# Kernel tuning notes

Measured on AMD Instinct MI355X. Metric: run time of the kernel, lower is better.

Reference implementation:

```python
import jax, jax.numpy as jnp
import numpy as np

IN_CH = 512
EMB = 512

def setup_inputs() -> dict:
    key = jax.random.key(0)
    ks = jax.random.split(key, 14)
    s = 0.02
    inp = {
        'input': jax.random.normal(ks[0], (8, IN_CH, 64, 64), jnp.float32),
        'context': jax.random.normal(ks[1], (8, EMB, 32, 32), jnp.float32),
        # proj_in: Conv2d(in_channels, emb_dim, 1) -> weight [emb, in_ch]
        'proj_in_w': jax.random.normal(ks[2], (EMB, IN_CH), jnp.float32) * s,
        'proj_in_b': jnp.zeros((EMB,), jnp.float32),
        # Linear weights stored as [in, out] (math-equivalent to torch [out,in].T)
        'wq_w': jax.random.normal(ks[3], (EMB, EMB), jnp.float32) * s,
        'wq_b': jnp.zeros((EMB,), jnp.float32),
        'wk_w': jax.random.normal(ks[4], (EMB, EMB), jnp.float32) * s,
        'wk_b': jnp.zeros((EMB,), jnp.float32),
        'wv_w': jax.random.normal(ks[5], (EMB, EMB), jnp.float32) * s,
        'wv_b': jnp.zeros((EMB,), jnp.float32),
        # proj_out: Conv2d(emb+in_ch, in_ch, 1) -> weight [in_ch, emb+in_ch]
        'proj_out_w': jax.random.normal(ks[6], (IN_CH, EMB + IN_CH), jnp.float32) * s,
        'proj_out_b': jnp.zeros((IN_CH,), jnp.float32),
    }
    return inp

def reference(input, context, proj_in_w, proj_in_b, wq_w, wq_b, wk_w, wk_b,
              wv_w, wv_b, proj_out_w, proj_out_b):
    b, c_in, h, w = input.shape
    _, c_ctx, hc, wc = context.shape
    scale = EMB ** (-0.5)

    # context: [b, emb, hc, wc] -> [b, L, emb]
    ctx = context.reshape(b, c_ctx, hc * wc).transpose(0, 2, 1)

    # proj_in (1x1 conv) + flatten: [b, in_ch, h, w] -> [b, hw, emb]
    x = jnp.einsum('bchw,ec->bhwe', input, proj_in_w) + proj_in_b
    x = x.reshape(b, h * w, EMB)

    Q = x @ wq_w + wq_b                 # [b, hw, emb]
    K = ctx @ wk_w + wk_b               # [b, L, emb]
    V = ctx @ wv_w + wv_b               # [b, L, emb]

    att = jnp.einsum('bid,bjd->bij', Q, K) * scale  # [b, hw, L]
    att = jax.nn.softmax(att, axis=-1)
    out = jnp.einsum('bij,bjd->bid', att, V)        # [b, hw, emb]

    # [b, hw, emb] -> [b, emb, h, w]
    out = out.reshape(b, h, w, EMB).transpose(0, 3, 1, 2)
    out = jnp.concatenate([input, out], axis=1)     # [b, in_ch+emb, h, w]
    out = jnp.einsum('bchw,oc->bohw', out, proj_out_w) + proj_out_b[None, :, None, None]
    return out
```

## Files before the change

### kernel.cpp

```cpp
#include <hip/hip_runtime.h>
#include <hip/hip_bf16.h>

using bf16 = __hip_bfloat16;
typedef short s16x8 __attribute__((ext_vector_type(8)));
typedef float f32x4 __attribute__((ext_vector_type(4)));
typedef unsigned short u16;

__device__ __forceinline__ void gld_lds16(const void* g, void* l) {
  __builtin_amdgcn_global_load_lds(
      (const __attribute__((address_space(1))) void*)g,
      (__attribute__((address_space(3))) void*)l, 16, 0, 0);
}

__device__ __forceinline__ float bf2f(u16 u) {
  unsigned int x = ((unsigned int)u) << 16;
  return __builtin_bit_cast(float, x);
}

__global__ __launch_bounds__(256) void convert_f32_bf16(
    const float* __restrict__ in, bf16* __restrict__ out, int n) {
  int i = blockIdx.x * 256 + threadIdx.x;
  if (i < n) out[i] = __float2bfloat16(in[i]);
}

__global__ __launch_bounds__(256) void zero_f32(float* __restrict__ p, int n) {
  int i = blockIdx.x * 256 + threadIdx.x;
  if (i < n) p[i] = 0.f;
}

__global__ __launch_bounds__(256) void transpose_f32_to_bf16(
    const float* __restrict__ in, bf16* __restrict__ out, int inner,
    long in_b, long out_b, int out_ld, int coloff) {
  __shared__ float tile[32][33];
  const int bx = blockIdx.x;
  const int by = blockIdx.y;
  const int bz = blockIdx.z;
  const int tx = threadIdx.x & 31;
  const int ty = threadIdx.x >> 5;
  const float* ib = in + (long)bz * in_b;
  bf16* ob = out + (long)bz * out_b;
#pragma unroll
  for (int i = 0; i < 4; ++i) {
    int r = ty + i * 8;
    tile[r][tx] = ib[(long)(by * 32 + r) * inner + bx * 32 + tx];
  }
  __syncthreads();
#pragma unroll
  for (int i = 0; i < 4; ++i) {
    int r = ty + i * 8;
    ob[(long)(bx * 32 + r) * out_ld + coloff + by * 32 + tx] =
        __float2bfloat16(tile[tx][r]);
  }
}

__global__ __launch_bounds__(256) void transpose_w4(
    const float* __restrict__ w0, const float* __restrict__ w1,
    const float* __restrict__ w2, const float* __restrict__ w3,
    bf16* __restrict__ o0, bf16* __restrict__ o1,
    bf16* __restrict__ o2, bf16* __restrict__ o3) {
  __shared__ float tile[32][33];
  const float* in;
  bf16* out;
  switch (blockIdx.z) {
    case 0: in = w0; out = o0; break;
    case 1: in = w1; out = o1; break;
    case 2: in = w2; out = o2; break;
    default: in = w3; out = o3; break;
  }
  const int bx = blockIdx.x, by = blockIdx.y;
  const int tx = threadIdx.x & 31, ty = threadIdx.x >> 5;
#pragma unroll
  for (int i = 0; i < 4; ++i) {
    int r = ty + i * 8;
    tile[r][tx] = in[(long)(by * 32 + r) * 512 + bx * 32 + tx];
  }
  __syncthreads();
#pragma unroll
  for (int i = 0; i < 4; ++i) {
    int r = ty + i * 8;
    out[(long)(bx * 32 + r) * 512 + by * 32 + tx] = __float2bfloat16(tile[tx][r]);
  }
}

__global__ __launch_bounds__(256) void bias_combine(
    const float* __restrict__ pb, const float* __restrict__ wq,
    const float* __restrict__ qb, float* __restrict__ out) {
  int o = blockIdx.x * 256 + threadIdx.x;
  if (o >= 512) return;
  float s = qb[o];
  for (int e = 0; e < 512; ++e) s += pb[e] * wq[e * 512 + o];
  out[o] = s;
}

template <int OUT_BF16, int BIAS_MODE, int EPI>
__global__ __launch_bounds__(256, 4) void gemm_bt_kernel(
    const bf16* __restrict__ A, long sAb, int lda,
    const bf16* __restrict__ B, long sBb, int ldb,
    void* __restrict__ Cp, long sCb, int ldc,
    const float* __restrict__ bias, float* __restrict__ sc, long scb,
    float alpha, int K, int lgx, int lgy) {
  __shared__ __align__(16) bf16 tA[128 * 64];
  __shared__ __align__(16) bf16 tB[128 * 64];

  const int nwg = gridDim.x;
  const int orig = blockIdx.x;
  const int q = nwg >> 3, r = nwg & 7;
  const int xcd = orig & 7, local = orig >> 3;
  const int wgid = (xcd < r ? xcd * (q + 1) : r * (q + 1) + (xcd - r) * q) + local;
  const int bn = wgid & ((1 << lgx) - 1);
  const int tmp = wgid >> lgx;
  const int bm = tmp & ((1 << lgy) - 1);
  const int bz = tmp >> lgy;

  const int t = threadIdx.x;
  const int w = t >> 6;
  const int lane = t & 63;

  const bf16* Ab = A + (long)bz * sAb;
  const bf16* Bb = B + (long)bz * sBb;

  const int srow = t >> 3;
  const int scol = ((t & 7) ^ (srow & 7)) * 8;
  const long a_base = (long)(bm * 128 + srow) * lda + scol;
  const long b_base = (long)(bn * 128 + srow) * ldb + scol;
  char* lA = (char*)tA + w * 1024;
  char* lB = (char*)tB + w * 1024;

  const int wr = w >> 1, wc = w & 1;
  const int r15 = lane & 15;
  const int khalf = lane >> 4;
  f32x4 acc[4][4] = {};

  for (int kt = 0; kt < K; kt += 64) {
#pragma unroll
    for (int i = 0; i < 4; ++i) {
      gld_lds16(Ab + a_base + (long)(i * 32) * lda + kt, lA + i * 4096);
      gld_lds16(Bb + b_base + (long)(i * 32) * ldb + kt, lB + i * 4096);
    }
    __syncthreads();
#pragma unroll
    for (int kk = 0; kk < 2; ++kk) {
      const int chunk = kk * 4 + khalf;
      s16x8 af[4], bg[4];
#pragma unroll
      for (int m = 0; m < 4; ++m) {
        const int row = wr * 64 + m * 16 + r15;
        af[m] = *(const s16x8*)(tA + row * 64 + ((chunk ^ (row & 7)) * 8));
      }
#pragma unroll
      for (int n = 0; n < 4; ++n) {
        const int row = wc * 64 + n * 16 + r15;
        bg[n] = *(const s16x8*)(tB + row * 64 + ((chunk ^ (row & 7)) * 8));
      }
#pragma unroll
      for (int m = 0; m < 4; ++m)
#pragma unroll
        for (int n = 0; n < 4; ++n)
          acc[m][n] = __builtin_amdgcn_mfma_f32_16x16x32_bf16(af[m], bg[n],
                                                              acc[m][n], 0, 0, 0);
    }
    __syncthreads();
  }

#pragma unroll
  for (int m = 0; m < 4; ++m) {
    const int rb = bm * 128 + wr * 64 + m * 16 + (lane >> 4) * 4;
    float rin[4];
    if (EPI == 2) {
#pragma unroll
      for (int j = 0; j < 4; ++j) rin[j] = 1.0f / sc[(long)bz * scb + rb + j];
    }
    float rs[4] = {0.f, 0.f, 0.f, 0.f};
#pragma unroll
    for (int n = 0; n < 4; ++n) {
      const int col = bn * 128 + wc * 64 + n * 16 + r15;
      float bN = 0.f;
      if (BIAS_MODE == 1) bN = bias[col];
#pragma unroll
      for (int j = 0; j < 4; ++j) {
        const int row = rb + j;
        float v;
        if (EPI == 1) {
          v = __expf(acc[m][n][j] * alpha);
          rs[j] += v;
        } else if (EPI == 2) {
          v = acc[m][n][j] * rin[j];
        } else {
          v = acc[m][n][j] * alpha;
          if (BIAS_MODE == 1) v += bN;
          if (BIAS_MODE == 2) v += bias[row];
        }
        const long off = (long)bz * sCb + (long)row * ldc + col;
        if (OUT_BF16)
          ((bf16*)Cp)[off] = __float2bfloat16(v);
        else
          ((float*)Cp)[off] = v;
      }
    }
    if (EPI == 1) {
#pragma unroll
      for (int j = 0; j < 4; ++j) {
        float s = rs[j];
#pragma unroll
        for (int sh = 1; sh < 16; sh <<= 1) s += __shfl_xor(s, sh, 64);
        if (r15 == 0) atomicAdd(sc + (long)bz * scb + rb + j, s);
      }
    }
  }
}

template <int OUT_BF16, int BIAS_MODE, int EPI>
__global__ __launch_bounds__(512) void gemm256_kernel(
    const bf16* __restrict__ A, long sAb, int lda,
    const bf16* __restrict__ B, long sBb, int ldb,
    void* __restrict__ Cp, long sCb, int ldc,
    const float* __restrict__ bias, float* __restrict__ sc, long scb,
    float alpha, int K, int lgx, int lgy) {
  extern __shared__ __align__(16) char smem[];
  bf16* tA = (bf16*)smem;
  bf16* tB = (bf16*)(smem + 65536);

  const int nwg = gridDim.x;
  const int orig = blockIdx.x;
  const int q = nwg >> 3, r = nwg & 7;
  const int xcd = orig & 7, local = orig >> 3;
  const int wgid = (xcd < r ? xcd * (q + 1) : r * (q + 1) + (xcd - r) * q) + local;
  const int bn = wgid & ((1 << lgx) - 1);
  const int tmp = wgid >> lgx;
  const int bm = tmp & ((1 << lgy) - 1);
  const int bz = tmp >> lgy;

  const int t = threadIdx.x;
  const int w = t >> 6;
  const int lane = t & 63;
  const int wr = w >> 2, wc = w & 3;
  const int r15 = lane & 15;
  const int khalf = lane >> 4;

  const bf16* Ab = A + (long)bz * sAb;
  const bf16* Bb = B + (long)bz * sBb;

  const int srow = t >> 3;
  const int scol = ((t & 7) ^ (srow & 7)) * 8;
  const long a_base = (long)(bm * 256 + srow) * lda + scol;
  const long b_base = (long)(bn * 256 + srow) * ldb + scol;

  f32x4 acc[8][4] = {};

  auto STAGE = [&](int buf, int kt) {
    char* dA = (char*)(tA + buf * 16384) + w * 1024;
    char* dB = (char*)(tB + buf * 16384) + w * 1024;
#pragma unroll
    for (int i = 0; i < 4; ++i)
      gld_lds16(Ab + a_base + (long)(i * 64) * lda + kt, dA + i * 8192);
#pragma unroll
    for (int i = 0; i < 4; ++i)
      gld_lds16(Bb + b_base + (long)(i * 64) * ldb + kt, dB + i * 8192);
  };

  auto COMPUTE = [&](int buf) {
    const bf16* tAc = tA + buf * 16384;
    const bf16* tBc = tB + buf * 16384;
    s16x8 bg[2][4];
#pragma unroll
    for (int ks = 0; ks < 2; ++ks)
#pragma unroll
      for (int n = 0; n < 4; ++n) {
        const int row = wc * 64 + n * 16 + r15;
        bg[ks][n] =
            *(const s16x8*)(tBc + row * 64 + (((ks * 4 + khalf) ^ (row & 7)) * 8));
      }
#pragma unroll
    for (int m = 0; m < 8; ++m) {
      const int row = wr * 128 + m * 16 + r15;
      const s16x8 a0 =
          *(const s16x8*)(tAc + row * 64 + ((khalf ^ (row & 7)) * 8));
      const s16x8 a1 =
          *(const s16x8*)(tAc + row * 64 + (((4 + khalf) ^ (row & 7)) * 8));
#pragma unroll
      for (int n = 0; n < 4; ++n)
        acc[m][n] =
            __builtin_amdgcn_mfma_f32_16x16x32_bf16(a0, bg[0][n], acc[m][n], 0, 0, 0);
#pragma unroll
      for (int n = 0; n < 4; ++n)
        acc[m][n] =
            __builtin_amdgcn_mfma_f32_16x16x32_bf16(a1, bg[1][n], acc[m][n], 0, 0, 0);
    }
  };

  STAGE(0, 0);
  __syncthreads();
  int cur = 0;
  for (int kt = 64; kt < K; kt += 64) {
    STAGE(cur ^ 1, kt);
    COMPUTE(cur);
    __syncthreads();
    cur ^= 1;
  }
  COMPUTE(cur);

#pragma unroll
  for (int m = 0; m < 8; ++m) {
    const int rb = bm * 256 + wr * 128 + m * 16 + (lane >> 4) * 4;
    float rin[4];
    if (EPI == 2) {
#pragma unroll
      for (int j = 0; j < 4; ++j) rin[j] = 1.0f / sc[(long)bz * scb + rb + j];
    }
    float rs[4] = {0.f, 0.f, 0.f, 0.f};
#pragma unroll
    for (int n = 0; n < 4; ++n) {
      const int col = bn * 256 + wc * 64 + n * 16 + r15;
      float bN = 0.f;
      if (BIAS_MODE == 1) bN = bias[col];
#pragma unroll
      for (int j = 0; j < 4; ++j) {
        const int row = rb + j;
        float v;
        if (EPI == 1) {
          v = __expf(acc[m][n][j] * alpha);
          rs[j] += v;
        } else if (EPI == 2) {
          v = acc[m][n][j] * rin[j];
        } else {
          v = acc[m][n][j] * alpha;
          if (BIAS_MODE == 1) v += bN;
          if (BIAS_MODE == 2) v += bias[row];
        }
        const long off = (long)bz * sCb + (long)row * ldc + col;
        if (OUT_BF16)
          ((bf16*)Cp)[off] = __float2bfloat16(v);
        else
          ((float*)Cp)[off] = v;
      }
    }
    if (EPI == 1) {
#pragma unroll
      for (int j = 0; j < 4; ++j) {
        float s = rs[j];
#pragma unroll
        for (int sh = 1; sh < 16; sh <<= 1) s += __shfl_xor(s, sh, 64);
        if (r15 == 0) atomicAdd(sc + (long)bz * scb + rb + j, s);
      }
    }
  }
}

extern "C" void kernel_launch(void* const* d_in, const int* in_sizes, int n_in,
                              void* d_out, int out_size, void* d_ws, size_t ws_size,
                              hipStream_t stream) {
  const float* input   = (const float*)d_in[0];
  const float* context = (const float*)d_in[1];
  const float* pin_w   = (const float*)d_in[2];
  const float* pin_b   = (const float*)d_in[3];
  const float* wq_w    = (const float*)d_in[4];
  const float* wq_b    = (const float*)d_in[5];
  const float* wk_w    = (const float*)d_in[6];
  const float* wk_b    = (const float*)d_in[7];
  const float* wv_w    = (const float*)d_in[8];
  const float* wv_b    = (const float*)d_in[9];
  const float* pout_w  = (const float*)d_in[10];
  const float* pout_b  = (const float*)d_in[11];

  char* ws = (char*)d_ws;
  size_t off = 0;
  auto alloc = [&](size_t bytes) -> void* {
    void* p = ws + off;
    off += (bytes + 255) & ~(size_t)255;
    return p;
  };
  bf16* poutw = (bf16*)alloc((size_t)512 * 1024 * 2);
  bf16* wqT  = (bf16*)alloc((size_t)512 * 512 * 2);
  bf16* wkT  = (bf16*)alloc((size_t)512 * 512 * 2);
  bf16* wvT  = (bf16*)alloc((size_t)512 * 512 * 2);
  bf16* pinT = (bf16*)alloc((size_t)512 * 512 * 2);
  bf16* WQc  = (bf16*)alloc((size_t)512 * 512 * 2);
  float* bQc = (float*)alloc((size_t)512 * 4);
  bf16* cat  = (bf16*)alloc((size_t)32768 * 1024 * 2);
  bf16* ctxt = (bf16*)alloc((size_t)8192 * 512 * 2);
  bf16* Qb   = (bf16*)alloc((size_t)32768 * 512 * 2);
  bf16* Kmb  = (bf16*)alloc((size_t)8192 * 512 * 2);
  bf16* Vtb  = (bf16*)alloc((size_t)8 * 512 * 1024 * 2);
  bf16* Sb   = (bf16*)alloc((size_t)8 * 4096 * 1024 * 2);
  float* rsum = (float*)alloc((size_t)32768 * 4);

  dim3 blk(256);

  hipFuncSetAttribute((const void*)gemm256_kernel<1, 1, 0>,
                      hipFuncAttributeMaxDynamicSharedMemorySize, 131072);
  hipFuncSetAttribute((const void*)gemm256_kernel<1, 0, 1>,
                      hipFuncAttributeMaxDynamicSharedMemorySize, 131072);
  hipFuncSetAttribute((const void*)gemm256_kernel<1, 0, 2>,
                      hipFuncAttributeMaxDynamicSharedMemorySize, 131072);
  hipFuncSetAttribute((const void*)gemm256_kernel<0, 2, 0>,
                      hipFuncAttributeMaxDynamicSharedMemorySize, 131072);

  convert_f32_bf16<<<2048, blk, 0, stream>>>(pout_w, poutw, 512 * 1024);
  zero_f32<<<128, blk, 0, stream>>>(rsum, 32768);
  transpose_w4<<<dim3(16, 16, 4), blk, 0, stream>>>(wq_w, wk_w, wv_w, pin_w,
                                                    wqT, wkT, wvT, pinT);
  bias_combine<<<2, blk, 0, stream>>>(pin_b, wq_w, wq_b, bQc);
  transpose_f32_to_bf16<<<dim3(128, 16, 8), blk, 0, stream>>>(
      input, cat, 4096, (long)512 * 4096, (long)4096 * 1024, 1024, 0);
  transpose_f32_to_bf16<<<dim3(32, 16, 8), blk, 0, stream>>>(
      context, ctxt, 1024, (long)512 * 1024, (long)1024 * 512, 512, 0);

  const float scale = 0.04419417382415922f;

  gemm_bt_kernel<1, 0, 0><<<dim3(16), blk, 0, stream>>>(
      wqT, 0, 512, pinT, 0, 512, WQc, 0, 512, nullptr, nullptr, 0, 1.f, 512, 2, 2);
  gemm_bt_kernel<1, 1, 0><<<dim3(256), blk, 0, stream>>>(
      ctxt, 0, 512, wkT, 0, 512, Kmb, 0, 512, wk_b, nullptr, 0, 1.f, 512, 2, 6);
  gemm_bt_kernel<1, 2, 0><<<dim3(256), blk, 0, stream>>>(
      wvT, 0, 512, ctxt, (long)1024 * 512, 512, Vtb, (long)512 * 1024, 1024,
      wv_b, nullptr, 0, 1.f, 512, 3, 2);

  gemm256_kernel<1, 1, 0><<<dim3(256), dim3(512), 131072, stream>>>(
      cat, 0, 1024, WQc, 0, 512, Qb, 0, 512, bQc, nullptr, 0, 1.f, 512, 1, 7);
  gemm256_kernel<1, 0, 1><<<dim3(512), dim3(512), 131072, stream>>>(
      Qb, (long)4096 * 512, 512, Kmb, (long)1024 * 512, 512, Sb,
      (long)4096 * 1024, 1024, nullptr, rsum, 4096, scale, 512, 2, 4);
  gemm256_kernel<1, 0, 2><<<dim3(256), dim3(512), 131072, stream>>>(
      Sb, (long)4096 * 1024, 1024, Vtb, (long)512 * 1024, 1024,
      (void*)(cat + 512), (long)4096 * 1024, 1024, nullptr, rsum, 4096, 1.f,
      1024, 1, 4);
  gemm256_kernel<0, 2, 0><<<dim3(256), dim3(512), 131072, stream>>>(
      poutw, 0, 1024, cat, (long)4096 * 1024, 1024, d_out,
      (long)512 * 4096, 4096, pout_b, nullptr, 0, 1.f, 1024, 4, 1);
}
```

Measured before the change: 365.6 us.

## Pipeline 256x256 GEMM with split-K half stages and explicit vmcnt waits

Restructures the main 256x256 bf16 GEMM's main loop so each 64-wide K tile is staged as two 32-wide halves. Loads for the next halves are issued while the current half is computed, and explicit s_waitcnt vmcnt counts replace full __syncthreads drains. It also changes the LDS swizzle to a 32-column layout with one fragment load per MFMA group, raises MFMA wave priority with s_setprio, and adds launch_bounds min-blocks 2. The goal is to hide global-to-LDS latency behind MFMA work. The hand-tuned waitcnt counts and barrier placement are fragile and could hurt correctness or occupancy if they are wrong.

Result: slower. 388.2 us (+6.2%).

```diff
diff --git a/kernel.cpp b/kernel.cpp
--- a/kernel.cpp
+++ b/kernel.cpp
@@ -210,15 +210,13 @@
 }
 
 template <int OUT_BF16, int BIAS_MODE, int EPI>
-__global__ __launch_bounds__(512) void gemm256_kernel(
+__global__ __launch_bounds__(512, 2) void gemm256p_kernel(
     const bf16* __restrict__ A, long sAb, int lda,
     const bf16* __restrict__ B, long sBb, int ldb,
     void* __restrict__ Cp, long sCb, int ldc,
     const float* __restrict__ bias, float* __restrict__ sc, long scb,
     float alpha, int K, int lgx, int lgy) {
   extern __shared__ __align__(16) char smem[];
-  bf16* tA = (bf16*)smem;
-  bf16* tB = (bf16*)(smem + 65536);
 
   const int nwg = gridDim.x;
   const int orig = blockIdx.x;
@@ -232,76 +230,82 @@
 
   const int t = threadIdx.x;
   const int w = t >> 6;
-  const int lane = t & 63;
+  const int l = t & 63;
   const int wr = w >> 2, wc = w & 3;
-  const int r15 = lane & 15;
-  const int khalf = lane >> 4;
+  const int r15 = l & 15;
+  const int c0 = l >> 4;
+  const int frag_off = r15 * 64 + ((c0 ^ (r15 & 3)) << 4);
 
   const bf16* Ab = A + (long)bz * sAb;
   const bf16* Bb = B + (long)bz * sBb;
 
-  const int srow = t >> 3;
-  const int scol = ((t & 7) ^ (srow & 7)) * 8;
-  const long a_base = (long)(bm * 256 + srow) * lda + scol;
-  const long b_base = (long)(bn * 256 + srow) * ldb + scol;
+  const int st_row = w * 16 + (l >> 2);
+  const int st_col = ((l & 3) ^ ((l >> 2) & 3)) << 3;
+  const long a_r0 = (long)(bm * 256 + st_row);
+  const long b_r0 = (long)(bn * 256 + st_row);
 
   f32x4 acc[8][4] = {};
-
-  auto STAGE = [&](int buf, int kt) {
-    char* dA = (char*)(tA + buf * 16384) + w * 1024;
-    char* dB = (char*)(tB + buf * 16384) + w * 1024;
-#pragma unroll
-    for (int i = 0; i < 4; ++i)
-      gld_lds16(Ab + a_base + (long)(i * 64) * lda + kt, dA + i * 8192);
-#pragma unroll
-    for (int i = 0; i < 4; ++i)
-      gld_lds16(Bb + b_base + (long)(i * 64) * ldb + kt, dB + i * 8192);
+  const int T = K >> 6;
+
+  auto STAGE = [&](int tt, int ks, int b) {
+    const long kb = tt * 64 + ks * 32 + st_col;
+    char* dA = smem + b * 65536 + ks * 16384 + w * 1024;
+#pragma unroll
+    for (int i = 0; i < 2; ++i) {
+      gld_lds16(Ab + (a_r0 + i * 128) * lda + kb, dA + i * 8192);
+      gld_lds16(Bb + (b_r0 + i * 128) * ldb + kb, dA + 32768 + i * 8192);
+    }
   };
 
-  auto COMPUTE = [&](int buf) {
-    const bf16* tAc = tA + buf * 16384;
-    const bf16* tBc = tB + buf * 16384;
-    s16x8 bg[2][4];
-#pragma unroll
-    for (int ks = 0; ks < 2; ++ks)
-#pragma unroll
-      for (int n = 0; n < 4; ++n) {
-        const int row = wc * 64 + n * 16 + r15;
-        bg[ks][n] =
-            *(const s16x8*)(tBc + row * 64 + (((ks * 4 + khalf) ^ (row & 7)) * 8));
-      }
+  auto COMPUTE = [&](int b, int ks) {
+    const char* hA = smem + b * 65536 + ks * 16384;
+    const char* hB = hA + 32768;
+    s16x8 bg[4];
+#pragma unroll
+    for (int n = 0; n < 4; ++n)
+      bg[n] = *(const s16x8*)(hB + (wc * 64 + n * 16) * 64 + frag_off);
+    __builtin_amdgcn_s_setprio(1);
 #pragma unroll
     for (int m = 0; m < 8; ++m) {
-      const int row = wr * 128 + m * 16 + r15;
-      const s16x8 a0 =
-          *(const s16x8*)(tAc + row * 64 + ((khalf ^ (row & 7)) * 8));
-      const s16x8 a1 =
-          *(const s16x8*)(tAc + row * 64 + (((4 + khalf) ^ (row & 7)) * 8));
+      const s16x8 a = *(const s16x8*)(hA + (wr * 128 + m * 16) * 64 + frag_off);
 #pragma unroll
       for (int n = 0; n < 4; ++n)
-        acc[m][n] =
-            __builtin_amdgcn_mfma_f32_16x16x32_bf16(a0, bg[0][n], acc[m][n], 0, 0, 0);
-#pragma unroll
-      for (int n = 0; n < 4; ++n)
-        acc[m][n] =
-            __builtin_amdgcn_mfma_f32_16x16x32_bf16(a1, bg[1][n], acc[m][n], 0, 0, 0);
-    }
+        acc[m][n] = __builtin_amdgcn_mfma_f32_16x16x32_bf16(a, bg[n],
+                                                            acc[m][n], 0, 0, 0);
+    }
+    __builtin_amdgcn_s_setprio(0);
   };
 
-  STAGE(0, 0);
-  __syncthreads();
-  int cur = 0;
-  for (int kt = 64; kt < K; kt += 64) {
-    STAGE(cur ^ 1, kt);
-    COMPUTE(cur);
-    __syncthreads();
-    cur ^= 1;
-  }
-  COMPUTE(cur);
+  STAGE(0, 0, 0);
+  STAGE(0, 1, 0);
+  if (T > 1) STAGE(1, 0, 1);
+
+  for (int tt = 0; tt < T; ++tt) {
+    const int cb = tt & 1;
+    if (tt + 1 < T) STAGE(tt + 1, 1, cb ^ 1);
+    if (tt < T - 1) asm volatile("s_waitcnt vmcnt(12)" ::: "memory");
+    else            asm volatile("s_waitcnt vmcnt(4)" ::: "memory");
+    __builtin_amdgcn_s_barrier();
+    __builtin_amdgcn_sched_barrier(0);
+    COMPUTE(cb, 0);
+    asm volatile("s_waitcnt lgkmcnt(0)" ::: "memory");
+    __builtin_amdgcn_s_barrier();
+    __builtin_amdgcn_sched_barrier(0);
+    if (tt + 2 < T) STAGE(tt + 2, 0, cb);
+    if (tt < T - 2)       asm volatile("s_waitcnt vmcnt(12)" ::: "memory");
+    else if (tt == T - 2) asm volatile("s_waitcnt vmcnt(8)" ::: "memory");
+    else                  asm volatile("s_waitcnt vmcnt(0)" ::: "memory");
+    __builtin_amdgcn_s_barrier();
+    __builtin_amdgcn_sched_barrier(0);
+    COMPUTE(cb, 1);
+    asm volatile("s_waitcnt lgkmcnt(0)" ::: "memory");
+    __builtin_amdgcn_s_barrier();
+    __builtin_amdgcn_sched_barrier(0);
+  }
 
 #pragma unroll
   for (int m = 0; m < 8; ++m) {
-    const int rb = bm * 256 + wr * 128 + m * 16 + (lane >> 4) * 4;
+    const int rb = bm * 256 + wr * 128 + m * 16 + c0 * 4;
     float rin[4];
     if (EPI == 2) {
 #pragma unroll
@@ -386,13 +390,13 @@
 
   dim3 blk(256);
 
-  hipFuncSetAttribute((const void*)gemm256_kernel<1, 1, 0>,
+  hipFuncSetAttribute((const void*)gemm256p_kernel<1, 1, 0>,
                       hipFuncAttributeMaxDynamicSharedMemorySize, 131072);
-  hipFuncSetAttribute((const void*)gemm256_kernel<1, 0, 1>,
+  hipFuncSetAttribute((const void*)gemm256p_kernel<1, 0, 1>,
                       hipFuncAttributeMaxDynamicSharedMemorySize, 131072);
-  hipFuncSetAttribute((const void*)gemm256_kernel<1, 0, 2>,
+  hipFuncSetAttribute((const void*)gemm256p_kernel<1, 0, 2>,
                       hipFuncAttributeMaxDynamicSharedMemorySize, 131072);
-  hipFuncSetAttribute((const void*)gemm256_kernel<0, 2, 0>,
+  hipFuncSetAttribute((const void*)gemm256p_kernel<0, 2, 0>,
                       hipFuncAttributeMaxDynamicSharedMemorySize, 131072);
 
   convert_f32_bf16<<<2048, blk, 0, stream>>>(pout_w, poutw, 512 * 1024);
@@ -415,16 +419,16 @@
       wvT, 0, 512, ctxt, (long)1024 * 512, 512, Vtb, (long)512 * 1024, 1024,
       wv_b, nullptr, 0, 1.f, 512, 3, 2);
 
-  gemm256_kernel<1, 1, 0><<<dim3(256), dim3(512), 131072, stream>>>(
+  gemm256p_kernel<1, 1, 0><<<dim3(256), dim3(512), 131072, stream>>>(
       cat, 0, 1024, WQc, 0, 512, Qb, 0, 512, bQc, nullptr, 0, 1.f, 512, 1, 7);
-  gemm256_kernel<1, 0, 1><<<dim3(512), dim3(512), 131072, stream>>>(
+  gemm256p_kernel<1, 0, 1><<<dim3(512), dim3(512), 131072, stream>>>(
       Qb, (long)4096 * 512, 512, Kmb, (long)1024 * 512, 512, Sb,
       (long)4096 * 1024, 1024, nullptr, rsum, 4096, scale, 512, 2, 4);
-  gemm256_kernel<1, 0, 2><<<dim3(256), dim3(512), 131072, stream>>>(
+  gemm256p_kernel<1, 0, 2><<<dim3(256), dim3(512), 131072, stream>>>(
       Sb, (long)4096 * 1024, 1024, Vtb, (long)512 * 1024, 1024,
       (void*)(cat + 512), (long)4096 * 1024, 1024, nullptr, rsum, 4096, 1.f,
       1024, 1, 4);
-  gemm256_kernel<0, 2, 0><<<dim3(256), dim3(512), 131072, stream>>>(
+  gemm256p_kernel<0, 2, 0><<<dim3(256), dim3(512), 131072, stream>>>(
       poutw, 0, 1024, cat, (long)4096 * 1024, 1024, d_out,
       (long)512 * 4096, 4096, pout_b, nullptr, 0, 1.f, 1024, 4, 1);
 }
```
